# Kernel optimization log

Measured on AMD Instinct MI355X. Metric: run time of the kernel, lower is better.

## Reference

```python
import jax, jax.numpy as jnp
import numpy as np

N = 50000        # nodes
E_RND = 800000   # random edges (self-loops appended -> E = 850000)
IN = 256         # in_dim
H1, D = 4, 32    # heads[0], num_hidden
C = 40           # num_classes (heads[1] = 1)
SLOPE = 0.2      # leaky_relu negative_slope
EPS = 1e-5       # batchnorm eps


def setup_inputs() -> dict:
    key = jax.random.key(0)
    ks = jax.random.split(key, 9)
    x = jax.random.normal(ks[0], (N, IN), jnp.float32)
    loops = jnp.arange(N, dtype=jnp.int32)
    src = jnp.concatenate([jax.random.randint(ks[1], (E_RND,), 0, N, dtype=jnp.int32), loops])
    dst = jnp.concatenate([jax.random.randint(ks[2], (E_RND,), 0, N, dtype=jnp.int32), loops])
    glorot = lambda k, shape, fan: jax.random.normal(k, shape, jnp.float32) * np.float32(1.0 / np.sqrt(fan))
    W1 = glorot(ks[3], (IN, H1 * D), IN)
    al1 = glorot(ks[4], (H1, D), D)
    ar1 = glorot(ks[5], (H1, D), D)
    gamma = jnp.ones((H1 * D,), jnp.float32)
    beta = jnp.zeros((H1 * D,), jnp.float32)
    W2 = glorot(ks[6], (H1 * D, C), H1 * D)
    al2 = glorot(ks[7], (1, C), C)
    ar2 = glorot(ks[8], (1, C), C)
    return dict(x=x, src=src, dst=dst, W1=W1, al1=al1, ar1=ar1,
                gamma=gamma, beta=beta, W2=W2, al2=al2, ar2=ar2)


def _gat_conv(h, src, dst, W, al, ar, heads, out_dim):
    """DGL GATConv (eval mode: dropouts are identity, no residual/bias)."""
    n = h.shape[0]
    ft = (h @ W).reshape(n, heads, out_dim)              # (N,H,D)
    el = jnp.einsum('nhd,hd->nh', ft, al)                # (N,H)
    er = jnp.einsum('nhd,hd->nh', ft, ar)
    e = jax.nn.leaky_relu(el[src] + er[dst], SLOPE)      # (E,H)
    # edge softmax over incoming edges per destination node (stable)
    m = jax.ops.segment_max(e, dst, num_segments=n)
    m = jnp.where(jnp.isfinite(m), m, 0.0)
    ex = jnp.exp(e - m[dst])
    s = jax.ops.segment_sum(ex, dst, num_segments=n)
    a = ex / jnp.maximum(s[dst], 1e-9)                   # (E,H)
    msg = a[:, :, None] * ft[src]                        # (E,H,D)
    return jax.ops.segment_sum(msg, dst, num_segments=n) # (N,H,D)


def reference(x, src, dst, W1, al1, ar1, gamma, beta, W2, al2, ar2):
    h = _gat_conv(x, src, dst, W1, al1, ar1, H1, D).reshape(N, H1 * D)
    mu = jnp.mean(h, axis=0)
    var = jnp.var(h, axis=0)                              # biased var, as torch BN training
    h = (h - mu) * jax.lax.rsqrt(var + EPS) * gamma + beta
    h = jax.nn.elu(h)
    logits = _gat_conv(h, src, dst, W2, al2, ar2, 1, C).mean(axis=1)  # (N,C)
    return jax.nn.log_softmax(logits, axis=-1)
```

## Files before the change

kernel.cpp:

```cpp
#include <hip/hip_runtime.h>
#include <hip/hip_bf16.h>
#include <math.h>

#define N_NODES 50000
#define N_EDGES 850000
#define IN_DIM  256
#define HD      128
#define H1      4
#define D       32
#define NC      40
#define SLOPE   0.2f
#define EPS_BN  1e-5f

#define NBIN    782
#define BCAP    1536
#define NREP    32
#define RCAP    160
#define NWAVE   4

typedef __attribute__((ext_vector_type(8))) short bf16x8;
typedef __attribute__((ext_vector_type(4))) float f32x4;
typedef unsigned long long u64;

__device__ __forceinline__ unsigned short f2bf(float x) {
    union { float f; unsigned u; } v; v.f = x;
    unsigned r = v.u + 0x7FFF + ((v.u >> 16) & 1);
    return (unsigned short)(r >> 16);
}
__device__ __forceinline__ float bf2f(unsigned short h) {
    union { unsigned u; float f; } v; v.u = ((unsigned)h) << 16;
    return v.f;
}
__device__ __forceinline__ uint4 pack8(float a0,float a1,float a2,float a3,
                                       float a4,float a5,float a6,float a7) {
    uint4 p;
    p.x = f2bf(a0) | ((unsigned)f2bf(a1) << 16);
    p.y = f2bf(a2) | ((unsigned)f2bf(a3) << 16);
    p.z = f2bf(a4) | ((unsigned)f2bf(a5) << 16);
    p.w = f2bf(a6) | ((unsigned)f2bf(a7) << 16);
    return p;
}

__device__ __forceinline__ int tile32_addr(int row, int chunk) {
    return row * 32 + ((chunk ^ ((row >> 1) & 3)) << 3);
}

__global__ __launch_bounds__(256) void binscatter_k(const int* __restrict__ src,
                                                    const int* __restrict__ dst,
                                                    int* __restrict__ bincur,
                                                    unsigned* __restrict__ tmp,
                                                    const float* __restrict__ W1,
                                                    const float* __restrict__ W2,
                                                    unsigned short* __restrict__ W1t,
                                                    unsigned short* __restrict__ W2t) {
    int e = blockIdx.x * blockDim.x + threadIdx.x;
    if (e < IN_DIM * HD) {
        int k = e >> 7, n = e & 127;
        W1t[n * IN_DIM + k] = f2bf(W1[e]);
    }
    if (e < 48 * HD) {
        int n = e >> 7, k = e & 127;
        float v = (n < NC) ? W2[k * NC + n] : 0.f;
        W2t[e] = f2bf(v);
    }
    if (e >= N_EDGES) return;
    int v = dst[e];
    int b = v >> 6;
    int rep = blockIdx.x & (NREP - 1);
    int cell = b * NREP + rep;
    int cur = atomicAdd(&bincur[cell], 1);
    if (cur < RCAP)
        tmp[(size_t)cell * RCAP + cur] = ((unsigned)(v & 63) << 16) | (unsigned)src[e];
}

__global__ __launch_bounds__(256) void binsort_k(const unsigned* __restrict__ tmp,
                                                 const int* __restrict__ bincur,
                                                 unsigned* __restrict__ csrp,
                                                 u64* __restrict__ rowp,
                                                 int* __restrict__ bintot) {
    __shared__ int cnts[NREP];
    __shared__ int hist[64];
    __shared__ int cur[64];
    int b = blockIdx.x, tid = threadIdx.x;
    int nbase = b << 6;
    size_t cbase = (size_t)b * BCAP;
    int wv = tid >> 6, ln = tid & 63;
    if (tid < NREP) cnts[tid] = min(bincur[b * NREP + tid], RCAP);
    if (tid < 64) hist[tid] = 0;
    __syncthreads();
    for (int s = wv; s < NREP; s += NWAVE) {
        int c = cnts[s];
        const unsigned* seg = tmp + (size_t)(b * NREP + s) * RCAP;
        for (int t = ln; t < c; t += 64)
            atomicAdd(&hist[seg[t] >> 16], 1);
    }
    __syncthreads();
    if (tid < 64) {
        int h = hist[tid];
        int v = h;
        #pragma unroll
        for (int off = 1; off < 64; off <<= 1) {
            int t2 = __shfl_up(v, off);
            if (tid >= off) v += t2;
        }
        int excl = v - h;
        cur[tid] = excl;
        int node = nbase + tid;
        if (node < N_NODES)
            rowp[node] = ((u64)h << 32) | (unsigned)(cbase + excl);
        if (tid == 63) bintot[b] = v;
    }
    __syncthreads();
    for (int s = wv; s < NREP; s += NWAVE) {
        int c = cnts[s];
        const unsigned* seg = tmp + (size_t)(b * NREP + s) * RCAP;
        for (int t = ln; t < c; t += 64) {
            unsigned p = seg[t];
            int pos = atomicAdd(&cur[p >> 16], 1);
            csrp[cbase + pos] = p;
        }
    }
}

__global__ __launch_bounds__(256) void mfma1_k(const float* __restrict__ X,
                                               const unsigned short* __restrict__ W1t,
                                               unsigned short* __restrict__ ftb) {
    __shared__ unsigned short alds[2][64 * 32];
    __shared__ unsigned short wlds[2][128 * 32];
    const int tid = threadIdx.x;
    const int lane = tid & 63, wid = tid >> 6;
    const int wr = wid >> 1, wc = wid & 1;
    const int rowBase = blockIdx.x * 64;
    const int s_arow = tid >> 2, s_ac = tid & 3;
    const int s_wcol = tid >> 1, s_wc0 = (tid & 1) * 2;

    auto stageA = [&](int buf, int ks) {
        float4 v0 = make_float4(0.f,0.f,0.f,0.f), v1 = v0;
        int gr = rowBase + s_arow;
        if (gr < N_NODES) {
            const float4* p = (const float4*)(X + (size_t)gr * IN_DIM + ks * 32 + s_ac * 8);
            v0 = p[0]; v1 = p[1];
        }
        *(uint4*)&alds[buf][tile32_addr(s_arow, s_ac)] =
            pack8(v0.x,v0.y,v0.z,v0.w,v1.x,v1.y,v1.z,v1.w);
    };
    auto stageW = [&](int buf, int ks) {
        const uint4* g = (const uint4*)(W1t + s_wcol * IN_DIM + ks * 32 + s_wc0 * 8);
        uint4 a = g[0], b = g[1];
        *(uint4*)&wlds[buf][tile32_addr(s_wcol, s_wc0)] = a;
        *(uint4*)&wlds[buf][tile32_addr(s_wcol, s_wc0 + 1)] = b;
    };

    f32x4 acc[2][4];
    #pragma unroll
    for (int mf = 0; mf < 2; ++mf)
        #pragma unroll
        for (int nf = 0; nf < 4; ++nf)
            acc[mf][nf] = (f32x4){0.f, 0.f, 0.f, 0.f};

    stageA(0, 0); stageW(0, 0);
    for (int ks = 0; ks < 8; ++ks) {
        __syncthreads();
        if (ks < 7) { stageA((ks + 1) & 1, ks + 1); stageW((ks + 1) & 1, ks + 1); }
        int buf = ks & 1;
        bf16x8 afrag[2], bfrag[4];
        #pragma unroll
        for (int mf = 0; mf < 2; ++mf) {
            int row = wr * 32 + mf * 16 + (lane & 15);
            afrag[mf] = *(const bf16x8*)&alds[buf][tile32_addr(row, lane >> 4)];
        }
        #pragma unroll
        for (int nf = 0; nf < 4; ++nf) {
            int col = wc * 64 + nf * 16 + (lane & 15);
            bfrag[nf] = *(const bf16x8*)&wlds[buf][tile32_addr(col, lane >> 4)];
        }
        #pragma unroll
        for (int mf = 0; mf < 2; ++mf)
            #pragma unroll
            for (int nf = 0; nf < 4; ++nf)
                acc[mf][nf] = __builtin_amdgcn_mfma_f32_16x16x32_bf16(
                    afrag[mf], bfrag[nf], acc[mf][nf], 0, 0, 0);
    }
    #pragma unroll
    for (int mf = 0; mf < 2; ++mf) {
        int r0 = rowBase + wr * 32 + mf * 16 + (lane >> 4) * 4;
        #pragma unroll
        for (int nf = 0; nf < 4; ++nf) {
            int col = wc * 64 + nf * 16 + (lane & 15);
            #pragma unroll
            for (int v = 0; v < 4; ++v) {
                int r = r0 + v;
                if (r < N_NODES) ftb[(size_t)r * HD + col] = f2bf(acc[mf][nf][v]);
            }
        }
    }
}

__global__ __launch_bounds__(256) void mfma2_k(const unsigned short* __restrict__ Hin,
                                               const unsigned short* __restrict__ W2t,
                                               const float* __restrict__ bnsum,
                                               const float* __restrict__ bnsq,
                                               const float* __restrict__ gamma,
                                               const float* __restrict__ beta,
                                               unsigned short* __restrict__ ft2b) {
    __shared__ unsigned short alds[2][64 * 32];
    __shared__ unsigned short wlds[48 * 128];
    __shared__ float sc_lds[HD], sh_lds[HD];
    const int tid = threadIdx.x;
    const int lane = tid & 63, wid = tid >> 6;
    const int rowBase = blockIdx.x * 64;
    const int s_arow = tid >> 2, s_ac = tid & 3;

    if (tid < HD) {
        const float invN = 1.0f / (float)N_NODES;
        float mu = bnsum[tid] * invN;
        float var = bnsq[tid] * invN - mu * mu;
        float sc = gamma[tid] * rsqrtf(var + EPS_BN);
        sc_lds[tid] = sc;
        sh_lds[tid] = beta[tid] - mu * sc;
    }
    for (int i = tid; i < 48 * 16; i += 256) {
        int col = i >> 4, c = i & 15;
        uint4 v = *(const uint4*)(W2t + col * HD + c * 8);
        *(uint4*)&wlds[col * HD + ((c ^ (col & 7)) << 3)] = v;
    }
    __syncthreads();

    auto stageA = [&](int buf, int ks) {
        int c0 = ks * 32 + s_ac * 8;
        uint4 pv = make_uint4(0,0,0,0);
        int gr = rowBase + s_arow;
        if (gr < N_NODES) pv = *(const uint4*)(Hin + (size_t)gr * HD + c0);
        float4 sc0 = *(const float4*)(sc_lds + c0), sc1 = *(const float4*)(sc_lds + c0 + 4);
        float4 sh0 = *(const float4*)(sh_lds + c0), sh1 = *(const float4*)(sh_lds + c0 + 4);
        float t[8];
        t[0] = fmaf(bf2f(pv.x & 0xffff), sc0.x, sh0.x);
        t[1] = fmaf(bf2f(pv.x >> 16),    sc0.y, sh0.y);
        t[2] = fmaf(bf2f(pv.y & 0xffff), sc0.z, sh0.z);
        t[3] = fmaf(bf2f(pv.y >> 16),    sc0.w, sh0.w);
        t[4] = fmaf(bf2f(pv.z & 0xffff), sc1.x, sh1.x);
        t[5] = fmaf(bf2f(pv.z >> 16),    sc1.y, sh1.y);
        t[6] = fmaf(bf2f(pv.w & 0xffff), sc1.z, sh1.z);
        t[7] = fmaf(bf2f(pv.w >> 16),    sc1.w, sh1.w);
        #pragma unroll
        for (int i = 0; i < 8; ++i) t[i] = t[i] > 0.f ? t[i] : expm1f(t[i]);
        *(uint4*)&alds[buf][tile32_addr(s_arow, s_ac)] =
            pack8(t[0],t[1],t[2],t[3],t[4],t[5],t[6],t[7]);
    };

    f32x4 acc[3];
    #pragma unroll
    for (int nf = 0; nf < 3; ++nf) acc[nf] = (f32x4){0.f, 0.f, 0.f, 0.f};

    stageA(0, 0);
    for (int ks = 0; ks < 4; ++ks) {
        __syncthreads();
        if (ks < 3) stageA((ks + 1) & 1, ks + 1);
        int buf = ks & 1;
        int row = wid * 16 + (lane & 15);
        bf16x8 a = *(const bf16x8*)&alds[buf][tile32_addr(row, lane >> 4)];
        #pragma unroll
        for (int nf = 0; nf < 3; ++nf) {
            int col = nf * 16 + (lane & 15);
            int c = ks * 4 + (lane >> 4);
            bf16x8 b = *(const bf16x8*)&wlds[col * HD + ((c ^ (col & 7)) << 3)];
            acc[nf] = __builtin_amdgcn_mfma_f32_16x16x32_bf16(a, b, acc[nf], 0, 0, 0);
        }
    }
    int r0 = rowBase + wid * 16 + (lane >> 4) * 4;
    #pragma unroll
    for (int nf = 0; nf < 3; ++nf) {
        int col = nf * 16 + (lane & 15);
        if (col < NC) {
            #pragma unroll
            for (int v = 0; v < 4; ++v) {
                int r = r0 + v;
                if (r < N_NODES) ft2b[(size_t)r * NC + col] = f2bf(acc[nf][v]);
            }
        }
    }
}

__global__ void eler1b_k(const unsigned short* __restrict__ ftb,
                         const float* __restrict__ alw, const float* __restrict__ arw,
                         float* __restrict__ el, float* __restrict__ er) {
    int t = blockIdx.x * blockDim.x + threadIdx.x;
    if (t >= N_NODES * H1) return;
    int n = t >> 2, h = t & 3;
    const unsigned short* f = ftb + (size_t)n * HD + h * D;
    const float* a = alw + h * D;
    const float* r = arw + h * D;
    float sl = 0.f, sr = 0.f;
    #pragma unroll
    for (int d = 0; d < D; d += 8) {
        uint4 fv = *(const uint4*)(f + d);
        float x0 = bf2f(fv.x & 0xffff), x1 = bf2f(fv.x >> 16);
        float x2 = bf2f(fv.y & 0xffff), x3 = bf2f(fv.y >> 16);
        float x4 = bf2f(fv.z & 0xffff), x5 = bf2f(fv.z >> 16);
        float x6 = bf2f(fv.w & 0xffff), x7 = bf2f(fv.w >> 16);
        sl += x0*a[d] + x1*a[d+1] + x2*a[d+2] + x3*a[d+3]
            + x4*a[d+4] + x5*a[d+5] + x6*a[d+6] + x7*a[d+7];
        sr += x0*r[d] + x1*r[d+1] + x2*r[d+2] + x3*r[d+3]
            + x4*r[d+4] + x5*r[d+5] + x6*r[d+6] + x7*r[d+7];
    }
    el[t] = sl; er[t] = sr;
}

__global__ void eler2b_k(const unsigned short* __restrict__ ft2b,
                         const float* __restrict__ alw, const float* __restrict__ arw,
                         float* __restrict__ el, float* __restrict__ er) {
    int n = blockIdx.x * blockDim.x + threadIdx.x;
    if (n >= N_NODES) return;
    const unsigned short* f = ft2b + (size_t)n * NC;
    float sl = 0.f, sr = 0.f;
    #pragma unroll
    for (int d = 0; d < NC; d += 4) {
        uint2 fv = *(const uint2*)(f + d);
        float x0 = bf2f(fv.x & 0xffff), x1 = bf2f(fv.x >> 16);
        float x2 = bf2f(fv.y & 0xffff), x3 = bf2f(fv.y >> 16);
        sl += x0*alw[d] + x1*alw[d+1] + x2*alw[d+2] + x3*alw[d+3];
        sr += x0*arw[d] + x1*arw[d+1] + x2*arw[d+2] + x3*arw[d+3];
    }
    el[n] = sl; er[n] = sr;
}

__global__ void exw2_k(const unsigned* __restrict__ csrp,
                       const int* __restrict__ bintot,
                       const float* __restrict__ el, const float* __restrict__ er,
                       float* __restrict__ exw) {
    int s = blockIdx.x * blockDim.x + threadIdx.x;
    int b = s / BCAP;
    int off = s - b * BCAP;
    if (off >= bintot[b]) return;
    unsigned p = csrp[s];
    float t = el[p & 0xffff] + er[(b << 6) + (p >> 16)];
    t = t > 0.f ? t : SLOPE * t;
    exw[s] = __expf(t);
}

__global__ __launch_bounds__(256) void gather1_k(const u64* __restrict__ rowp,
                                                 const unsigned* __restrict__ csrp,
                                                 const float* __restrict__ el,
                                                 const float* __restrict__ er,
                                                 const unsigned short* __restrict__ ftb,
                                                 unsigned int* __restrict__ h1b) {
    int w = (blockIdx.x * blockDim.x + threadIdx.x) >> 6;
    if (w >= N_NODES) return;
    int lane = threadIdx.x & 63;
    int hh = lane >> 4;
    float erv = er[w * H1 + hh];
    u64 rp = rowp[w];
    int jb = (int)(rp & 0xffffffffu), je = jb + (int)(rp >> 32);
    float ax = 0.f, ay = 0.f, ssum = 0.f;
    int j = jb;
    for (; j + 7 < je; j += 8) {
        int u[8]; float wv[8]; ushort2 f[8];
        #pragma unroll
        for (int k = 0; k < 8; ++k) u[k] = csrp[j + k] & 0xffff;
        #pragma unroll
        for (int k = 0; k < 8; ++k)
            f[k] = *(const ushort2*)(ftb + (size_t)u[k] * HD + lane * 2);
        #pragma unroll
        for (int k = 0; k < 8; ++k) {
            float t = el[u[k] * H1 + hh] + erv;
            t = t > 0.f ? t : SLOPE * t;
            wv[k] = __expf(t);
        }
        #pragma unroll
        for (int k = 0; k < 8; ++k) {
            ax = fmaf(wv[k], bf2f(f[k].x), ax);
            ay = fmaf(wv[k], bf2f(f[k].y), ay);
            ssum += wv[k];
        }
    }
    for (; j < je; ++j) {
        int u0 = csrp[j] & 0xffff;
        float t = el[u0 * H1 + hh] + erv;
        t = t > 0.f ? t : SLOPE * t;
        float w0 = __expf(t);
        ushort2 f0 = *(const ushort2*)(ftb + (size_t)u0 * HD + lane * 2);
        ax = fmaf(w0, bf2f(f0.x), ax); ay = fmaf(w0, bf2f(f0.y), ay);
        ssum += w0;
    }
    float inv = 1.0f / fmaxf(ssum, 1e-9f);
    h1b[(size_t)w * 64 + lane] = (unsigned)f2bf(ax * inv)
                               | ((unsigned)f2bf(ay * inv) << 16);
}

__global__ void bnstats_k(const unsigned short* __restrict__ h1b,
                          float* __restrict__ sums, float* __restrict__ sumsq) {
    int c = threadIdx.x;
    float acc = 0.f, acc2 = 0.f;
    for (int r = blockIdx.x; r < N_NODES; r += gridDim.x) {
        float v = bf2f(h1b[(size_t)r * HD + c]);
        acc += v; acc2 += v * v;
    }
    atomicAdd(&sums[c], acc);
    atomicAdd(&sumsq[c], acc2);
}

__global__ __launch_bounds__(256) void gather2_k(const u64* __restrict__ rowp,
                                                 const unsigned* __restrict__ csrp,
                                                 const float* __restrict__ exw,
                                                 const unsigned short* __restrict__ ft2b,
                                                 float* __restrict__ out) {
    int w = (blockIdx.x * blockDim.x + threadIdx.x) >> 6;
    if (w >= N_NODES) return;
    int lane = threadIdx.x & 63;
    u64 rp = rowp[w];
    int jb = (int)(rp & 0xffffffffu), je = jb + (int)(rp >> 32);
    float acc = 0.f, ssum = 0.f;
    int j = jb;
    for (; j + 7 < je; j += 8) {
        int u[8]; float wv[8]; float fv[8];
        #pragma unroll
        for (int k = 0; k < 8; ++k) u[k] = csrp[j + k] & 0xffff;
        #pragma unroll
        for (int k = 0; k < 8; ++k)
            fv[k] = (lane < NC) ? bf2f(ft2b[(size_t)u[k] * NC + lane]) : 0.f;
        #pragma unroll
        for (int k = 0; k < 8; ++k) wv[k] = exw[j + k];
        #pragma unroll
        for (int k = 0; k < 8; ++k) {
            acc = fmaf(wv[k], fv[k], acc);
            ssum += wv[k];
        }
    }
    for (; j < je; ++j) {
        int u0 = csrp[j] & 0xffff;
        float w0 = exw[j];
        float fa = (lane < NC) ? bf2f(ft2b[(size_t)u0 * NC + lane]) : 0.f;
        acc = fmaf(w0, fa, acc);
        ssum += w0;
    }
    float v = acc / fmaxf(ssum, 1e-9f);
    float vv = (lane < NC) ? v : -INFINITY;
    float m = vv;
    #pragma unroll
    for (int off = 32; off; off >>= 1) m = fmaxf(m, __shfl_xor(m, off));
    float ex2 = (lane < NC) ? __expf(vv - m) : 0.f;
    float sum = ex2;
    #pragma unroll
    for (int off = 32; off; off >>= 1) sum += __shfl_xor(sum, off);
    if (lane < NC) out[(size_t)w * NC + lane] = vv - m - logf(sum);
}

extern "C" void kernel_launch(void* const* d_in, const int* in_sizes, int n_in,
                              void* d_out, int out_size, void* d_ws, size_t ws_size,
                              hipStream_t stream) {
    const float* x     = (const float*)d_in[0];
    const int*   src   = (const int*)  d_in[1];
    const int*   dst   = (const int*)  d_in[2];
    const float* W1    = (const float*)d_in[3];
    const float* al1   = (const float*)d_in[4];
    const float* ar1   = (const float*)d_in[5];
    const float* gamma = (const float*)d_in[6];
    const float* beta  = (const float*)d_in[7];
    const float* W2    = (const float*)d_in[8];
    const float* al2   = (const float*)d_in[9];
    const float* ar2   = (const float*)d_in[10];
    float* out = (float*)d_out;

    const size_t NSLOT = (size_t)NBIN * BCAP;
    const size_t NTMP  = (size_t)NBIN * NREP * RCAP;

    char* ws = (char*)d_ws;
    size_t o = 0;
    auto allocB = [&](size_t bytes) { void* p = ws + o; o += (bytes + 15) & ~15ull; return p; };
    int*   bincur = (int*)allocB((size_t)NBIN * NREP * 4);
    float* bnsum  = (float*)allocB(HD * 4);
    float* bnsq   = (float*)allocB(HD * 4);
    size_t zeroBytes = o;
    unsigned* tmp  = (unsigned*)allocB(NTMP * 4);
    unsigned* csrp = (unsigned*)allocB(NSLOT * 4);
    int*   bintot  = (int*)allocB(NBIN * 4);
    u64*   rowp    = (u64*)allocB((size_t)N_NODES * 8);
    float* exw2    = (float*)allocB(NSLOT * 4);
    unsigned short* w1t  = (unsigned short*)allocB((size_t)IN_DIM * HD * 2);
    unsigned short* w2t  = (unsigned short*)allocB((size_t)48 * HD * 2);
    unsigned short* ft1b = (unsigned short*)allocB((size_t)N_NODES * HD * 2);
    unsigned int*   h1b  = (unsigned int*)allocB((size_t)N_NODES * HD * 2);
    float* el1  = (float*)allocB(N_NODES * H1 * 4);
    float* er1  = (float*)allocB(N_NODES * H1 * 4);
    unsigned short* ft2b = (unsigned short*)allocB((size_t)N_NODES * NC * 2);
    float* el2  = (float*)allocB(N_NODES * 4);
    float* er2  = (float*)allocB(N_NODES * 4);

    hipMemsetAsync(d_ws, 0, zeroBytes, stream);

    const int NB_E = (N_EDGES + 255) / 256;
    const int NB_G = (N_NODES + 63) / 64;
    const int NB_S = (int)(NSLOT / 256);

    binscatter_k<<<NB_E, 256, 0, stream>>>(src, dst, bincur, tmp, W1, W2, w1t, w2t);
    binsort_k<<<NBIN, 256, 0, stream>>>(tmp, bincur, csrp, rowp, bintot);

    mfma1_k<<<NB_G, 256, 0, stream>>>(x, w1t, ft1b);
    eler1b_k<<<(N_NODES * H1 + 255) / 256, 256, 0, stream>>>(ft1b, al1, ar1, el1, er1);
    gather1_k<<<N_NODES / 4, 256, 0, stream>>>(rowp, csrp, el1, er1, ft1b, h1b);

    bnstats_k<<<512, HD, 0, stream>>>((const unsigned short*)h1b, bnsum, bnsq);

    mfma2_k<<<NB_G, 256, 0, stream>>>((const unsigned short*)h1b, w2t,
                                      bnsum, bnsq, gamma, beta, ft2b);
    eler2b_k<<<(N_NODES + 255) / 256, 256, 0, stream>>>(ft2b, al2, ar2, el2, er2);
    exw2_k<<<NB_S, 256, 0, stream>>>(csrp, bintot, el2, er2, exw2);
    gather2_k<<<N_NODES / 4, 256, 0, stream>>>(rowp, csrp, exw2, ft2b, out);
}
```

Measured before the change: 358.5 us.

## Fuse attention-logit dots into GEMM epilogues and merge edge binning with GEMM1

Computes el/er directly from the MFMA accumulators in both GEMM kernels using 16-lane shuffle reductions, which removes the separate eler kernels and their re-read of the bf16 features. Edge binning is merged into the first GEMM launch as extra blocks, so scatter and matmul run concurrently. Weight conversion and zeroing of the counters and BN accumulators move into a small kernel that replaces the memset. The el/er values now come from fp32 accumulators rather than rounded bf16, which slightly changes numerics. Mixing block types in one launch may also affect occupancy because the edge blocks still reserve LDS.

New measurement: 328.5 us. 8.4% less time.

```diff
diff --git a/kernel.cpp b/kernel.cpp
--- a/kernel.cpp
+++ b/kernel.cpp
@@ -17,6 +17,8 @@
 #define NREP    32
 #define RCAP    160
 #define NWAVE   4
+#define NB_G    782
+#define NB_E    3321
 
 typedef __attribute__((ext_vector_type(8))) short bf16x8;
 typedef __attribute__((ext_vector_type(4))) float f32x4;
@@ -45,32 +47,149 @@
     return row * 32 + ((chunk ^ ((row >> 1) & 3)) << 3);
 }
 
-__global__ __launch_bounds__(256) void binscatter_k(const int* __restrict__ src,
-                                                    const int* __restrict__ dst,
-                                                    int* __restrict__ bincur,
-                                                    unsigned* __restrict__ tmp,
-                                                    const float* __restrict__ W1,
-                                                    const float* __restrict__ W2,
-                                                    unsigned short* __restrict__ W1t,
-                                                    unsigned short* __restrict__ W2t) {
-    int e = blockIdx.x * blockDim.x + threadIdx.x;
-    if (e < IN_DIM * HD) {
-        int k = e >> 7, n = e & 127;
-        W1t[n * IN_DIM + k] = f2bf(W1[e]);
-    }
-    if (e < 48 * HD) {
-        int n = e >> 7, k = e & 127;
+__global__ void cvtw0_k(const float* __restrict__ W1, const float* __restrict__ W2,
+                        unsigned short* __restrict__ W1t, unsigned short* __restrict__ W2t,
+                        int* __restrict__ bincur, float* __restrict__ bnsum,
+                        float* __restrict__ bnsq) {
+    int id = blockIdx.x * blockDim.x + threadIdx.x;
+    if (id < IN_DIM * HD) {
+        int k = id >> 7, n = id & 127;
+        W1t[n * IN_DIM + k] = f2bf(W1[id]);
+    }
+    if (id < 48 * HD) {
+        int n = id >> 7, k = id & 127;
         float v = (n < NC) ? W2[k * NC + n] : 0.f;
-        W2t[e] = f2bf(v);
-    }
-    if (e >= N_EDGES) return;
-    int v = dst[e];
-    int b = v >> 6;
-    int rep = blockIdx.x & (NREP - 1);
-    int cell = b * NREP + rep;
-    int cur = atomicAdd(&bincur[cell], 1);
-    if (cur < RCAP)
-        tmp[(size_t)cell * RCAP + cur] = ((unsigned)(v & 63) << 16) | (unsigned)src[e];
+        W2t[id] = f2bf(v);
+    }
+    if (id < NBIN * NREP) bincur[id] = 0;
+    if (id < HD) { bnsum[id] = 0.f; bnsq[id] = 0.f; }
+}
+
+__global__ __launch_bounds__(256) void fusedA_k(const float* __restrict__ X,
+                                                const unsigned short* __restrict__ W1t,
+                                                const float* __restrict__ al1,
+                                                const float* __restrict__ ar1,
+                                                unsigned short* __restrict__ ftb,
+                                                float* __restrict__ el,
+                                                float* __restrict__ er,
+                                                const int* __restrict__ src,
+                                                const int* __restrict__ dst,
+                                                int* __restrict__ bincur,
+                                                unsigned* __restrict__ tmp) {
+    __shared__ unsigned short alds[2][64 * 32];
+    __shared__ unsigned short wlds[2][128 * 32];
+
+    if (blockIdx.x >= NB_G) {
+        int bb = blockIdx.x - NB_G;
+        int e = bb * 256 + threadIdx.x;
+        if (e >= N_EDGES) return;
+        int v = dst[e];
+        int b = v >> 6;
+        int rep = bb & (NREP - 1);
+        int cell = b * NREP + rep;
+        int cur = atomicAdd(&bincur[cell], 1);
+        if (cur < RCAP)
+            tmp[(size_t)cell * RCAP + cur] = ((unsigned)(v & 63) << 16) | (unsigned)src[e];
+        return;
+    }
+
+    const int tid = threadIdx.x;
+    const int lane = tid & 63, wid = tid >> 6;
+    const int wr = wid >> 1, wc = wid & 1;
+    const int rowBase = blockIdx.x * 64;
+    const int s_arow = tid >> 2, s_ac = tid & 3;
+    const int s_wcol = tid >> 1, s_wc0 = (tid & 1) * 2;
+
+    auto stageA = [&](int buf, int ks) {
+        float4 v0 = make_float4(0.f,0.f,0.f,0.f), v1 = v0;
+        int gr = rowBase + s_arow;
+        if (gr < N_NODES) {
+            const float4* p = (const float4*)(X + (size_t)gr * IN_DIM + ks * 32 + s_ac * 8);
+            v0 = p[0]; v1 = p[1];
+        }
+        *(uint4*)&alds[buf][tile32_addr(s_arow, s_ac)] =
+            pack8(v0.x,v0.y,v0.z,v0.w,v1.x,v1.y,v1.z,v1.w);
+    };
+    auto stageW = [&](int buf, int ks) {
+        const uint4* g = (const uint4*)(W1t + s_wcol * IN_DIM + ks * 32 + s_wc0 * 8);
+        uint4 a = g[0], b = g[1];
+        *(uint4*)&wlds[buf][tile32_addr(s_wcol, s_wc0)] = a;
+        *(uint4*)&wlds[buf][tile32_addr(s_wcol, s_wc0 + 1)] = b;
+    };
+
+    f32x4 acc[2][4];
+    #pragma unroll
+    for (int mf = 0; mf < 2; ++mf)
+        #pragma unroll
+        for (int nf = 0; nf < 4; ++nf)
+            acc[mf][nf] = (f32x4){0.f, 0.f, 0.f, 0.f};
+
+    stageA(0, 0); stageW(0, 0);
+    for (int ks = 0; ks < 8; ++ks) {
+        __syncthreads();
+        if (ks < 7) { stageA((ks + 1) & 1, ks + 1); stageW((ks + 1) & 1, ks + 1); }
+        int buf = ks & 1;
+        bf16x8 afrag[2], bfrag[4];
+        #pragma unroll
+        for (int mf = 0; mf < 2; ++mf) {
+            int row = wr * 32 + mf * 16 + (lane & 15);
+            afrag[mf] = *(const bf16x8*)&alds[buf][tile32_addr(row, lane >> 4)];
+        }
+        #pragma unroll
+        for (int nf = 0; nf < 4; ++nf) {
+            int col = wc * 64 + nf * 16 + (lane & 15);
+            bfrag[nf] = *(const bf16x8*)&wlds[buf][tile32_addr(col, lane >> 4)];
+        }
+        #pragma unroll
+        for (int mf = 0; mf < 2; ++mf)
+            #pragma unroll
+            for (int nf = 0; nf < 4; ++nf)
+                acc[mf][nf] = __builtin_amdgcn_mfma_f32_16x16x32_bf16(
+                    afrag[mf], bfrag[nf], acc[mf][nf], 0, 0, 0);
+    }
+    #pragma unroll
+    for (int mf = 0; mf < 2; ++mf) {
+        int r0 = rowBase + wr * 32 + mf * 16 + (lane >> 4) * 4;
+        #pragma unroll
+        for (int nf = 0; nf < 4; ++nf) {
+            int col = wc * 64 + nf * 16 + (lane & 15);
+            #pragma unroll
+            for (int v = 0; v < 4; ++v) {
+                int r = r0 + v;
+                if (r < N_NODES) ftb[(size_t)r * HD + col] = f2bf(acc[mf][nf][v]);
+            }
+        }
+    }
+    float alw[4], arw[4];
+    #pragma unroll
+    for (int nf = 0; nf < 4; ++nf) {
+        int col = wc * 64 + nf * 16 + (lane & 15);
+        alw[nf] = al1[(col >> 5) * D + (col & 31)];
+        arw[nf] = ar1[(col >> 5) * D + (col & 31)];
+    }
+    #pragma unroll
+    for (int mf = 0; mf < 2; ++mf) {
+        #pragma unroll
+        for (int v = 0; v < 4; ++v) {
+            int r = rowBase + wr * 32 + mf * 16 + (lane >> 4) * 4 + v;
+            float elA = acc[mf][0][v] * alw[0] + acc[mf][1][v] * alw[1];
+            float erA = acc[mf][0][v] * arw[0] + acc[mf][1][v] * arw[1];
+            float elB = acc[mf][2][v] * alw[2] + acc[mf][3][v] * alw[3];
+            float erB = acc[mf][2][v] * arw[2] + acc[mf][3][v] * arw[3];
+            #pragma unroll
+            for (int off = 1; off < 16; off <<= 1) {
+                elA += __shfl_xor(elA, off, 16);
+                erA += __shfl_xor(erA, off, 16);
+                elB += __shfl_xor(elB, off, 16);
+                erB += __shfl_xor(erB, off, 16);
+            }
+            if ((lane & 15) == 0 && r < N_NODES) {
+                int hA = wc * 2;
+                el[r * H1 + hA]     = elA;  er[r * H1 + hA]     = erA;
+                el[r * H1 + hA + 1] = elB;  er[r * H1 + hA + 1] = erB;
+            }
+        }
+    }
 }
 
 __global__ __launch_bounds__(256) void binsort_k(const unsigned* __restrict__ tmp,
@@ -122,87 +241,17 @@
     }
 }
 
-__global__ __launch_bounds__(256) void mfma1_k(const float* __restrict__ X,
-                                               const unsigned short* __restrict__ W1t,
-                                               unsigned short* __restrict__ ftb) {
-    __shared__ unsigned short alds[2][64 * 32];
-    __shared__ unsigned short wlds[2][128 * 32];
-    const int tid = threadIdx.x;
-    const int lane = tid & 63, wid = tid >> 6;
-    const int wr = wid >> 1, wc = wid & 1;
-    const int rowBase = blockIdx.x * 64;
-    const int s_arow = tid >> 2, s_ac = tid & 3;
-    const int s_wcol = tid >> 1, s_wc0 = (tid & 1) * 2;
-
-    auto stageA = [&](int buf, int ks) {
-        float4 v0 = make_float4(0.f,0.f,0.f,0.f), v1 = v0;
-        int gr = rowBase + s_arow;
-        if (gr < N_NODES) {
-            const float4* p = (const float4*)(X + (size_t)gr * IN_DIM + ks * 32 + s_ac * 8);
-            v0 = p[0]; v1 = p[1];
-        }
-        *(uint4*)&alds[buf][tile32_addr(s_arow, s_ac)] =
-            pack8(v0.x,v0.y,v0.z,v0.w,v1.x,v1.y,v1.z,v1.w);
-    };
-    auto stageW = [&](int buf, int ks) {
-        const uint4* g = (const uint4*)(W1t + s_wcol * IN_DIM + ks * 32 + s_wc0 * 8);
-        uint4 a = g[0], b = g[1];
-        *(uint4*)&wlds[buf][tile32_addr(s_wcol, s_wc0)] = a;
-        *(uint4*)&wlds[buf][tile32_addr(s_wcol, s_wc0 + 1)] = b;
-    };
-
-    f32x4 acc[2][4];
-    #pragma unroll
-    for (int mf = 0; mf < 2; ++mf)
-        #pragma unroll
-        for (int nf = 0; nf < 4; ++nf)
-            acc[mf][nf] = (f32x4){0.f, 0.f, 0.f, 0.f};
-
-    stageA(0, 0); stageW(0, 0);
-    for (int ks = 0; ks < 8; ++ks) {
-        __syncthreads();
-        if (ks < 7) { stageA((ks + 1) & 1, ks + 1); stageW((ks + 1) & 1, ks + 1); }
-        int buf = ks & 1;
-        bf16x8 afrag[2], bfrag[4];
-        #pragma unroll
-        for (int mf = 0; mf < 2; ++mf) {
-            int row = wr * 32 + mf * 16 + (lane & 15);
-            afrag[mf] = *(const bf16x8*)&alds[buf][tile32_addr(row, lane >> 4)];
-        }
-        #pragma unroll
-        for (int nf = 0; nf < 4; ++nf) {
-            int col = wc * 64 + nf * 16 + (lane & 15);
-            bfrag[nf] = *(const bf16x8*)&wlds[buf][tile32_addr(col, lane >> 4)];
-        }
-        #pragma unroll
-        for (int mf = 0; mf < 2; ++mf)
-            #pragma unroll
-            for (int nf = 0; nf < 4; ++nf)
-                acc[mf][nf] = __builtin_amdgcn_mfma_f32_16x16x32_bf16(
-                    afrag[mf], bfrag[nf], acc[mf][nf], 0, 0, 0);
-    }
-    #pragma unroll
-    for (int mf = 0; mf < 2; ++mf) {
-        int r0 = rowBase + wr * 32 + mf * 16 + (lane >> 4) * 4;
-        #pragma unroll
-        for (int nf = 0; nf < 4; ++nf) {
-            int col = wc * 64 + nf * 16 + (lane & 15);
-            #pragma unroll
-            for (int v = 0; v < 4; ++v) {
-                int r = r0 + v;
-                if (r < N_NODES) ftb[(size_t)r * HD + col] = f2bf(acc[mf][nf][v]);
-            }
-        }
-    }
-}
-
 __global__ __launch_bounds__(256) void mfma2_k(const unsigned short* __restrict__ Hin,
                                                const unsigned short* __restrict__ W2t,
                                                const float* __restrict__ bnsum,
                                                const float* __restrict__ bnsq,
                                                const float* __restrict__ gamma,
                                                const float* __restrict__ beta,
-                                               unsigned short* __restrict__ ft2b) {
+                                               const float* __restrict__ al2,
+                                               const float* __restrict__ ar2,
+                                               unsigned short* __restrict__ ft2b,
+                                               float* __restrict__ el2,
+                                               float* __restrict__ er2) {
     __shared__ unsigned short alds[2][64 * 32];
     __shared__ unsigned short wlds[48 * 128];
     __shared__ float sc_lds[HD], sh_lds[HD];
@@ -279,49 +328,25 @@
             }
         }
     }
-}
-
-__global__ void eler1b_k(const unsigned short* __restrict__ ftb,
-                         const float* __restrict__ alw, const float* __restrict__ arw,
-                         float* __restrict__ el, float* __restrict__ er) {
-    int t = blockIdx.x * blockDim.x + threadIdx.x;
-    if (t >= N_NODES * H1) return;
-    int n = t >> 2, h = t & 3;
-    const unsigned short* f = ftb + (size_t)n * HD + h * D;
-    const float* a = alw + h * D;
-    const float* r = arw + h * D;
-    float sl = 0.f, sr = 0.f;
-    #pragma unroll
-    for (int d = 0; d < D; d += 8) {
-        uint4 fv = *(const uint4*)(f + d);
-        float x0 = bf2f(fv.x & 0xffff), x1 = bf2f(fv.x >> 16);
-        float x2 = bf2f(fv.y & 0xffff), x3 = bf2f(fv.y >> 16);
-        float x4 = bf2f(fv.z & 0xffff), x5 = bf2f(fv.z >> 16);
-        float x6 = bf2f(fv.w & 0xffff), x7 = bf2f(fv.w >> 16);
-        sl += x0*a[d] + x1*a[d+1] + x2*a[d+2] + x3*a[d+3]
-            + x4*a[d+4] + x5*a[d+5] + x6*a[d+6] + x7*a[d+7];
-        sr += x0*r[d] + x1*r[d+1] + x2*r[d+2] + x3*r[d+3]
-            + x4*r[d+4] + x5*r[d+5] + x6*r[d+6] + x7*r[d+7];
-    }
-    el[t] = sl; er[t] = sr;
-}
-
-__global__ void eler2b_k(const unsigned short* __restrict__ ft2b,
-                         const float* __restrict__ alw, const float* __restrict__ arw,
-                         float* __restrict__ el, float* __restrict__ er) {
-    int n = blockIdx.x * blockDim.x + threadIdx.x;
-    if (n >= N_NODES) return;
-    const unsigned short* f = ft2b + (size_t)n * NC;
-    float sl = 0.f, sr = 0.f;
-    #pragma unroll
-    for (int d = 0; d < NC; d += 4) {
-        uint2 fv = *(const uint2*)(f + d);
-        float x0 = bf2f(fv.x & 0xffff), x1 = bf2f(fv.x >> 16);
-        float x2 = bf2f(fv.y & 0xffff), x3 = bf2f(fv.y >> 16);
-        sl += x0*alw[d] + x1*alw[d+1] + x2*alw[d+2] + x3*alw[d+3];
-        sr += x0*arw[d] + x1*arw[d+1] + x2*arw[d+2] + x3*arw[d+3];
-    }
-    el[n] = sl; er[n] = sr;
+    float alw2[3], arw2[3];
+    #pragma unroll
+    for (int nf = 0; nf < 3; ++nf) {
+        int col = nf * 16 + (lane & 15);
+        alw2[nf] = (col < NC) ? al2[col] : 0.f;
+        arw2[nf] = (col < NC) ? ar2[col] : 0.f;
+    }
+    #pragma unroll
+    for (int v = 0; v < 4; ++v) {
+        int r = r0 + v;
+        float e_l = acc[0][v] * alw2[0] + acc[1][v] * alw2[1] + acc[2][v] * alw2[2];
+        float e_r = acc[0][v] * arw2[0] + acc[1][v] * arw2[1] + acc[2][v] * arw2[2];
+        #pragma unroll
+        for (int off = 1; off < 16; off <<= 1) {
+            e_l += __shfl_xor(e_l, off, 16);
+            e_r += __shfl_xor(e_r, off, 16);
+        }
+        if ((lane & 15) == 0 && r < N_NODES) { el2[r] = e_l; er2[r] = e_r; }
+    }
 }
 
 __global__ void exw2_k(const unsigned* __restrict__ csrp,
@@ -470,7 +495,6 @@
     int*   bincur = (int*)allocB((size_t)NBIN * NREP * 4);
     float* bnsum  = (float*)allocB(HD * 4);
     float* bnsq   = (float*)allocB(HD * 4);
-    size_t zeroBytes = o;
     unsigned* tmp  = (unsigned*)allocB(NTMP * 4);
     unsigned* csrp = (unsigned*)allocB(NSLOT * 4);
     int*   bintot  = (int*)allocB(NBIN * 4);
@@ -486,24 +510,20 @@
     float* el2  = (float*)allocB(N_NODES * 4);
     float* er2  = (float*)allocB(N_NODES * 4);
 
-    hipMemsetAsync(d_ws, 0, zeroBytes, stream);
-
-    const int NB_E = (N_EDGES + 255) / 256;
-    const int NB_G = (N_NODES + 63) / 64;
     const int NB_S = (int)(NSLOT / 256);
 
-    binscatter_k<<<NB_E, 256, 0, stream>>>(src, dst, bincur, tmp, W1, W2, w1t, w2t);
+    cvtw0_k<<<(IN_DIM * HD + 255) / 256, 256, 0, stream>>>(W1, W2, w1t, w2t,
+                                                           bincur, bnsum, bnsq);
+    fusedA_k<<<NB_G + NB_E, 256, 0, stream>>>(x, w1t, al1, ar1, ft1b, el1, er1,
+                                              src, dst, bincur, tmp);
     binsort_k<<<NBIN, 256, 0, stream>>>(tmp, bincur, csrp, rowp, bintot);
 
-    mfma1_k<<<NB_G, 256, 0, stream>>>(x, w1t, ft1b);
-    eler1b_k<<<(N_NODES * H1 + 255) / 256, 256, 0, stream>>>(ft1b, al1, ar1, el1, er1);
     gather1_k<<<N_NODES / 4, 256, 0, stream>>>(rowp, csrp, el1, er1, ft1b, h1b);
-
     bnstats_k<<<512, HD, 0, stream>>>((const unsigned short*)h1b, bnsum, bnsq);
 
     mfma2_k<<<NB_G, 256, 0, stream>>>((const unsigned short*)h1b, w2t,
-                                      bnsum, bnsq, gamma, beta, ft2b);
-    eler2b_k<<<(N_NODES + 255) / 256, 256, 0, stream>>>(ft2b, al2, ar2, el2, er2);
+                                      bnsum, bnsq, gamma, beta, al2, ar2,
+                                      ft2b, el2, er2);
     exw2_k<<<NB_S, 256, 0, stream>>>(csrp, bintot, el2, er2, exw2);
     gather2_k<<<N_NODES / 4, 256, 0, stream>>>(rowp, csrp, exw2, ft2b, out);
 }
```
